# Kernel optimization log

Measured on AMD Instinct MI355X. Metric: run time of the kernel, lower is better.

Reference implementation:

```python
import jax, jax.numpy as jnp
import numpy as np

B, S, D, H = 2, 2048, 1024, 16
DK = D // H


def setup_inputs() -> dict:
    key = jax.random.key(0)
    ks = jax.random.split(key, 11)
    s = 1.0 / np.sqrt(D)
    inp = {
        "q": jax.random.normal(ks[0], (B, S, D), jnp.float32),
        "k": jax.random.normal(ks[1], (B, S, D), jnp.float32),
        "v": jax.random.normal(ks[2], (B, S, D), jnp.float32),
        "mask": jnp.tril(jnp.ones((S, S), jnp.int32))[None, None],  # causal [1,1,S,S]
        "w_q": jax.random.normal(ks[3], (D, D), jnp.float32) * s,
        "b_q": jax.random.normal(ks[4], (D,), jnp.float32) * 0.01,
        "w_k": jax.random.normal(ks[5], (D, D), jnp.float32) * s,
        "b_k": jax.random.normal(ks[6], (D,), jnp.float32) * 0.01,
        "w_v": jax.random.normal(ks[7], (D, D), jnp.float32) * s,
        "b_v": jax.random.normal(ks[8], (D,), jnp.float32) * 0.01,
        "w_o": jax.random.normal(ks[9], (D, D), jnp.float32) * s,
        "b_o": jax.random.normal(ks[10], (D,), jnp.float32) * 0.01,
    }
    return inp


def reference(q, k, v, mask, w_q, b_q, w_k, b_k, w_v, b_v, w_o, b_o):
    # Linear projections (torch Linear: x @ W.T + b)
    query = q @ w_q.T + b_q  # [B,S,D]
    key_ = k @ w_k.T + b_k
    value = v @ w_v.T + b_v
    # split heads -> [B,H,S,DK]
    def split(x):
        return x.reshape(B, S, H, DK).transpose(0, 2, 1, 3)
    qh, kh, vh = split(query), split(key_), split(value)
    scores = jnp.einsum("bhqd,bhkd->bhqk", qh, kh) / jnp.sqrt(jnp.float32(DK))
    scores = jnp.where(mask == 0, jnp.float32(-1e9), scores)
    attn = jax.nn.softmax(scores, axis=-1)
    out = jnp.einsum("bhqk,bhkd->bhqd", attn, vh)  # [B,H,S,DK]
    out = out.transpose(0, 2, 1, 3).reshape(B, S, D)
    return out @ w_o.T + b_o
```

## Files before the change

kernel.cpp:

```cpp
#include <hip/hip_runtime.h>


typedef __attribute__((ext_vector_type(8))) short bf16x8;
typedef __attribute__((ext_vector_type(4))) float floatx4;
typedef __attribute__((ext_vector_type(4))) unsigned short u16x4;

#define S_LEN 2048
#define D_MODEL 1024
#define N_HEADS 16
#define D_HEAD 64
#define M_ROWS 4096
#define QSCALE 0.18033688011112042f

__device__ __forceinline__ unsigned short f32_to_bf16(float f) {
  unsigned int u = __builtin_bit_cast(unsigned int, f);
  u += 0x7FFFu + ((u >> 16) & 1u);
  return (unsigned short)(u >> 16);
}

__global__ __launch_bounds__(256) void cvt_w(
    const float* __restrict__ w0, const float* __restrict__ w1,
    const float* __restrict__ w2, const float* __restrict__ w3,
    unsigned short* __restrict__ dst) {
  const int z = blockIdx.y;
  const float* src = (z == 0) ? w0 : (z == 1) ? w1 : (z == 2) ? w2 : w3;
  unsigned short* d = dst + ((long)z << 20);
  const int n4 = 1 << 18;
  for (int i = blockIdx.x * 256 + threadIdx.x; i < n4; i += gridDim.x * 256) {
    float4 f = ((const float4*)src)[i];
    u16x4 o;
    o[0] = f32_to_bf16(f.x); o[1] = f32_to_bf16(f.y);
    o[2] = f32_to_bf16(f.z); o[3] = f32_to_bf16(f.w);
    ((u16x4*)d)[i] = o;
  }
}

__global__ __launch_bounds__(256) void cvt_x(
    const float* __restrict__ x0, const float* __restrict__ x1,
    const float* __restrict__ x2, unsigned short* __restrict__ dst) {
  const int z = blockIdx.y;
  const float* src = (z == 0) ? x0 : (z == 1) ? x1 : x2;
  unsigned short* d = dst + (long)z * M_ROWS * D_MODEL;
  const int n4 = (M_ROWS * D_MODEL) / 4;
  for (int i = blockIdx.x * 256 + threadIdx.x; i < n4; i += gridDim.x * 256) {
    float4 f = ((const float4*)src)[i];
    u16x4 o;
    o[0] = f32_to_bf16(f.x); o[1] = f32_to_bf16(f.y);
    o[2] = f32_to_bf16(f.z); o[3] = f32_to_bf16(f.w);
    ((u16x4*)d)[i] = o;
  }
}

#define GK 1024
#define GN 1024
#define LDP 72

template <bool XPRE>
__global__ __launch_bounds__(256, 3) void qkv_gemm(
    const float* __restrict__ Xq, const float* __restrict__ Xk, const float* __restrict__ Xv,
    const unsigned short* __restrict__ Xb,
    const unsigned short* __restrict__ Wb,
    const float* __restrict__ bq, const float* __restrict__ bk, const float* __restrict__ bv,
    unsigned short* __restrict__ Yq, unsigned short* __restrict__ Yk,
    unsigned short* __restrict__ Yvt) {
  __shared__ __align__(16) unsigned short As[128 * LDP];
  __shared__ __align__(16) unsigned short Bs[128 * LDP];

  const int z = blockIdx.z;
  const unsigned short* W = Wb + ((long)z << 20);
  const float* bias = (z == 0) ? bq : ((z == 1) ? bk : bv);

  const int r0 = blockIdx.x * 128;
  const int n0 = blockIdx.y * 128;
  const int tid = threadIdx.x;
  const int lane = tid & 63;
  const int wave = tid >> 6;
  const int quad = lane >> 4;
  const int ln = lane & 15;
  const int wm = (wave >> 1) * 64;
  const int wn = (wave & 1) * 64;

  floatx4 acc[4][4];
#pragma unroll
  for (int i = 0; i < 4; i++)
#pragma unroll
    for (int j = 0; j < 4; j++) acc[i][j] = (floatx4){0.f, 0.f, 0.f, 0.f};

  const int srow = tid >> 1;
  const int scol = (tid & 1) * 32;
  unsigned short* Asw = As + srow * LDP + scol;
  unsigned short* Bsw = Bs + srow * LDP + scol;
  const unsigned short* Bp = W + (long)(n0 + srow) * GK + scol;
  const float* ApF = nullptr;
  const unsigned short* ApH = nullptr;
  if constexpr (XPRE) {
    ApH = Xb + (long)z * M_ROWS * D_MODEL + (long)(r0 + srow) * GK + scol;
  } else {
    const float* X = (z == 0) ? Xq : ((z == 1) ? Xk : Xv);
    ApF = X + (long)(r0 + srow) * GK + scol;
  }

  for (int k0 = 0; k0 < GK; k0 += 64) {
    float4 b0 = *(const float4*)(Bp + k0);
    float4 b1 = *(const float4*)(Bp + k0 + 8);
    float4 b2 = *(const float4*)(Bp + k0 + 16);
    float4 b3 = *(const float4*)(Bp + k0 + 24);
    float4 a0, a1, a2, a3;
    if constexpr (XPRE) {
      a0 = *(const float4*)(ApH + k0);
      a1 = *(const float4*)(ApH + k0 + 8);
      a2 = *(const float4*)(ApH + k0 + 16);
      a3 = *(const float4*)(ApH + k0 + 24);
    } else {
      unsigned short ua[32] __attribute__((aligned(16)));
      float fa[32] __attribute__((aligned(16)));
#pragma unroll
      for (int c = 0; c < 8; c++)
        *(float4*)(fa + c * 4) = *(const float4*)(ApF + k0 + c * 4);
#pragma unroll
      for (int j = 0; j < 32; j++) ua[j] = f32_to_bf16(fa[j]);
      a0 = *(float4*)(ua); a1 = *(float4*)(ua + 8);
      a2 = *(float4*)(ua + 16); a3 = *(float4*)(ua + 24);
    }
    __syncthreads();
    *(float4*)(Asw) = a0;      *(float4*)(Asw + 8) = a1;
    *(float4*)(Asw + 16) = a2; *(float4*)(Asw + 24) = a3;
    *(float4*)(Bsw) = b0;      *(float4*)(Bsw + 8) = b1;
    *(float4*)(Bsw + 16) = b2; *(float4*)(Bsw + 24) = b3;
    __syncthreads();

#pragma unroll
    for (int ks = 0; ks < 64; ks += 32) {
      bf16x8 af[4], bfr[4];
#pragma unroll
      for (int mt = 0; mt < 4; mt++)
        af[mt] = *(const bf16x8*)(As + (wm + mt * 16 + ln) * LDP + ks + quad * 8);
#pragma unroll
      for (int nt = 0; nt < 4; nt++)
        bfr[nt] = *(const bf16x8*)(Bs + (wn + nt * 16 + ln) * LDP + ks + quad * 8);
#pragma unroll
      for (int mt = 0; mt < 4; mt++)
#pragma unroll
        for (int nt = 0; nt < 4; nt++)
          acc[mt][nt] = __builtin_amdgcn_mfma_f32_16x16x32_bf16(af[mt], bfr[nt], acc[mt][nt], 0, 0, 0);
    }
  }

#pragma unroll
  for (int nt = 0; nt < 4; nt++) {
    const int n = n0 + wn + nt * 16 + ln;
    const float bv = bias[n];
#pragma unroll
    for (int mt = 0; mt < 4; mt++) {
      const int r = r0 + wm + mt * 16 + quad * 4;
      if (z == 2) {
        u16x4 pk;
#pragma unroll
        for (int reg = 0; reg < 4; reg++) pk[reg] = f32_to_bf16(acc[mt][nt][reg] + bv);
        *(u16x4*)(Yvt + (long)n * M_ROWS + r) = pk;
      } else if (z == 0) {
#pragma unroll
        for (int reg = 0; reg < 4; reg++)
          Yq[(long)(r + reg) * GN + n] = f32_to_bf16((acc[mt][nt][reg] + bv) * QSCALE);
      } else {
#pragma unroll
        for (int reg = 0; reg < 4; reg++)
          Yk[(long)(r + reg) * GN + n] = f32_to_bf16(acc[mt][nt][reg] + bv);
      }
    }
  }
}

__global__ __launch_bounds__(256, 3) void out_gemm(
    const unsigned short* __restrict__ X,
    const unsigned short* __restrict__ W,
    const float* __restrict__ bias,
    float* __restrict__ Y) {
  __shared__ __align__(16) unsigned short As[64 * LDP];
  __shared__ __align__(16) unsigned short Bs[128 * LDP];

  const int r0 = blockIdx.x * 64;
  const int n0 = blockIdx.y * 128;
  const int tid = threadIdx.x;
  const int lane = tid & 63;
  const int wave = tid >> 6;
  const int quad = lane >> 4;
  const int ln = lane & 15;
  const int wm = (wave >> 1) * 32;
  const int wn = (wave & 1) * 64;

  floatx4 acc[2][4];
#pragma unroll
  for (int i = 0; i < 2; i++)
#pragma unroll
    for (int j = 0; j < 4; j++) acc[i][j] = (floatx4){0.f, 0.f, 0.f, 0.f};

  const int arow = tid >> 2;
  const int acol = (tid & 3) * 16;
  const unsigned short* Ap = X + (long)(r0 + arow) * GK + acol;
  unsigned short* Asw = As + arow * LDP + acol;
  const int brow = tid >> 1;
  const int bcol = (tid & 1) * 32;
  const unsigned short* Bp = W + (long)(n0 + brow) * GK + bcol;
  unsigned short* Bsw = Bs + brow * LDP + bcol;

  for (int k0 = 0; k0 < GK; k0 += 64) {
    float4 a0 = *(const float4*)(Ap + k0);
    float4 a1 = *(const float4*)(Ap + k0 + 8);
    float4 b0 = *(const float4*)(Bp + k0);
    float4 b1 = *(const float4*)(Bp + k0 + 8);
    float4 b2 = *(const float4*)(Bp + k0 + 16);
    float4 b3 = *(const float4*)(Bp + k0 + 24);
    __syncthreads();
    *(float4*)(Asw) = a0;      *(float4*)(Asw + 8) = a1;
    *(float4*)(Bsw) = b0;      *(float4*)(Bsw + 8) = b1;
    *(float4*)(Bsw + 16) = b2; *(float4*)(Bsw + 24) = b3;
    __syncthreads();

#pragma unroll
    for (int ks = 0; ks < 64; ks += 32) {
      bf16x8 af[2], bfr[4];
#pragma unroll
      for (int mt = 0; mt < 2; mt++)
        af[mt] = *(const bf16x8*)(As + (wm + mt * 16 + ln) * LDP + ks + quad * 8);
#pragma unroll
      for (int nt = 0; nt < 4; nt++)
        bfr[nt] = *(const bf16x8*)(Bs + (wn + nt * 16 + ln) * LDP + ks + quad * 8);
#pragma unroll
      for (int mt = 0; mt < 2; mt++)
#pragma unroll
        for (int nt = 0; nt < 4; nt++)
          acc[mt][nt] = __builtin_amdgcn_mfma_f32_16x16x32_bf16(af[mt], bfr[nt], acc[mt][nt], 0, 0, 0);
    }
  }

#pragma unroll
  for (int nt = 0; nt < 4; nt++) {
    const int n = n0 + wn + nt * 16 + ln;
    const float bv = bias[n];
#pragma unroll
    for (int mt = 0; mt < 2; mt++) {
      const int r = r0 + wm + mt * 16 + quad * 4;
#pragma unroll
      for (int reg = 0; reg < 4; reg++)
        Y[(long)(r + reg) * GN + n] = acc[mt][nt][reg] + bv;
    }
  }
}

#define PSTR 72

__global__ __launch_bounds__(64, 2) void attn_causal(
    const unsigned short* __restrict__ Q,
    const unsigned short* __restrict__ K,
    const unsigned short* __restrict__ Vt,
    unsigned short* __restrict__ O) {
  __shared__ __align__(16) unsigned short PbA[16 * PSTR];
  __shared__ __align__(16) unsigned short PbB[16 * PSTR];

  const int bh = blockIdx.x;
  const int pr = blockIdx.y;
  const int b = bh >> 4;
  const int h = bh & 15;

  const int lane = threadIdx.x;
  const int quad = lane >> 4;
  const int ln = lane & 15;

  const int s1 = pr, s2 = 127 - pr;
  const int q0A = s1 * 16, q0B = s2 * 16;
  const int nkt1 = (s1 >> 2) + 1;
  const int nkt2 = (s2 >> 2) + 1;

  const unsigned short* Qb = Q + (long)b * S_LEN * D_MODEL + h * D_HEAD;
  const unsigned short* Kb = K + (long)b * S_LEN * D_MODEL + h * D_HEAD;
  const unsigned short* Vb = Vt + (long)h * D_HEAD * M_ROWS + b * S_LEN;

  bf16x8 qfA[2], qfB[2];
  qfA[0] = *(const bf16x8*)(Qb + (long)(q0A + ln) * D_MODEL + quad * 8);
  qfA[1] = *(const bf16x8*)(Qb + (long)(q0A + ln) * D_MODEL + 32 + quad * 8);
  qfB[0] = *(const bf16x8*)(Qb + (long)(q0B + ln) * D_MODEL + quad * 8);
  qfB[1] = *(const bf16x8*)(Qb + (long)(q0B + ln) * D_MODEL + 32 + quad * 8);

  float mA = -1e30f, lA = 0.f, mB = -1e30f, lB = 0.f;
  floatx4 oA[4], oB[4];
#pragma unroll
  for (int nt = 0; nt < 4; nt++) {
    oA[nt] = (floatx4){0.f, 0.f, 0.f, 0.f};
    oB[nt] = (floatx4){0.f, 0.f, 0.f, 0.f};
  }

  auto loadKV = [&](bf16x8 (&kf)[4][2], bf16x8 (&vf)[4][2], int kt) {
    const int kv0 = kt * 64;
#pragma unroll
    for (int ct = 0; ct < 4; ct++) {
      const unsigned short* kp = Kb + (long)(kv0 + ct * 16 + ln) * D_MODEL + quad * 8;
      kf[ct][0] = *(const bf16x8*)(kp);
      kf[ct][1] = *(const bf16x8*)(kp + 32);
      const unsigned short* vp = Vb + (long)(ct * 16 + ln) * M_ROWS + kv0 + quad * 8;
      vf[ct][0] = *(const bf16x8*)(vp);
      vf[ct][1] = *(const bf16x8*)(vp + 32);
    }
  };

  auto iter = [&](bf16x8 (&kf)[4][2], bf16x8 (&vf)[4][2], int kt) {
    const int kv0 = kt * 64;
    const bool aAct = (kt < nkt1);

    floatx4 sB[4], sA[4];
#pragma unroll
    for (int ct = 0; ct < 4; ct++) {
      sB[ct] = (floatx4){0.f, 0.f, 0.f, 0.f};
      sB[ct] = __builtin_amdgcn_mfma_f32_16x16x32_bf16(kf[ct][0], qfB[0], sB[ct], 0, 0, 0);
      sB[ct] = __builtin_amdgcn_mfma_f32_16x16x32_bf16(kf[ct][1], qfB[1], sB[ct], 0, 0, 0);
    }
    if (aAct) {
#pragma unroll
      for (int ct = 0; ct < 4; ct++) {
        sA[ct] = (floatx4){0.f, 0.f, 0.f, 0.f};
        sA[ct] = __builtin_amdgcn_mfma_f32_16x16x32_bf16(kf[ct][0], qfA[0], sA[ct], 0, 0, 0);
        sA[ct] = __builtin_amdgcn_mfma_f32_16x16x32_bf16(kf[ct][1], qfA[1], sA[ct], 0, 0, 0);
      }
    }

    {
      float tmax = -1e30f;
      if (kt == nkt2 - 1) {
        const int qg = q0B + ln;
#pragma unroll
        for (int ct = 0; ct < 4; ct++) {
          const int kvb = kv0 + ct * 16 + quad * 4;
#pragma unroll
          for (int reg = 0; reg < 4; reg++) {
            float sv = sB[ct][reg];
            if (kvb + reg > qg) sv = -1e30f;
            sB[ct][reg] = sv;
            tmax = fmaxf(tmax, sv);
          }
        }
      } else {
#pragma unroll
        for (int ct = 0; ct < 4; ct++)
#pragma unroll
          for (int reg = 0; reg < 4; reg++) tmax = fmaxf(tmax, sB[ct][reg]);
      }
      tmax = fmaxf(tmax, __shfl_xor(tmax, 16, 64));
      tmax = fmaxf(tmax, __shfl_xor(tmax, 32, 64));
      const float mnew = fmaxf(mB, tmax);
      const float alpha = exp2f(mB - mnew);
      mB = mnew;
      float rsum = 0.f;
#pragma unroll
      for (int ct = 0; ct < 4; ct++) {
        u16x4 pk;
#pragma unroll
        for (int reg = 0; reg < 4; reg++) {
          const float p = exp2f(sB[ct][reg] - mB);
          rsum += p;
          pk[reg] = f32_to_bf16(p);
        }
        *(u16x4*)(PbB + ln * PSTR + ct * 16 + quad * 4) = pk;
      }
      rsum += __shfl_xor(rsum, 16, 64);
      rsum += __shfl_xor(rsum, 32, 64);
      lB = lB * alpha + rsum;
#pragma unroll
      for (int nt = 0; nt < 4; nt++)
#pragma unroll
        for (int reg = 0; reg < 4; reg++) oB[nt][reg] *= alpha;
    }

    if (aAct) {
      float tmax = -1e30f;
      if (kt == nkt1 - 1) {
        const int qg = q0A + ln;
#pragma unroll
        for (int ct = 0; ct < 4; ct++) {
          const int kvb = kv0 + ct * 16 + quad * 4;
#pragma unroll
          for (int reg = 0; reg < 4; reg++) {
            float sv = sA[ct][reg];
            if (kvb + reg > qg) sv = -1e30f;
            sA[ct][reg] = sv;
            tmax = fmaxf(tmax, sv);
          }
        }
      } else {
#pragma unroll
        for (int ct = 0; ct < 4; ct++)
#pragma unroll
          for (int reg = 0; reg < 4; reg++) tmax = fmaxf(tmax, sA[ct][reg]);
      }
      tmax = fmaxf(tmax, __shfl_xor(tmax, 16, 64));
      tmax = fmaxf(tmax, __shfl_xor(tmax, 32, 64));
      const float mnew = fmaxf(mA, tmax);
      const float alpha = exp2f(mA - mnew);
      mA = mnew;
      float rsum = 0.f;
#pragma unroll
      for (int ct = 0; ct < 4; ct++) {
        u16x4 pk;
#pragma unroll
        for (int reg = 0; reg < 4; reg++) {
          const float p = exp2f(sA[ct][reg] - mA);
          rsum += p;
          pk[reg] = f32_to_bf16(p);
        }
        *(u16x4*)(PbA + ln * PSTR + ct * 16 + quad * 4) = pk;
      }
      rsum += __shfl_xor(rsum, 16, 64);
      rsum += __shfl_xor(rsum, 32, 64);
      lA = lA * alpha + rsum;
#pragma unroll
      for (int nt = 0; nt < 4; nt++)
#pragma unroll
        for (int reg = 0; reg < 4; reg++) oA[nt][reg] *= alpha;
    }

    __builtin_amdgcn_wave_barrier();

    {
      bf16x8 p0 = *(const bf16x8*)(PbB + ln * PSTR + quad * 8);
      bf16x8 p1 = *(const bf16x8*)(PbB + ln * PSTR + 32 + quad * 8);
#pragma unroll
      for (int nt = 0; nt < 4; nt++) {
        oB[nt] = __builtin_amdgcn_mfma_f32_16x16x32_bf16(vf[nt][0], p0, oB[nt], 0, 0, 0);
        oB[nt] = __builtin_amdgcn_mfma_f32_16x16x32_bf16(vf[nt][1], p1, oB[nt], 0, 0, 0);
      }
    }
    if (aAct) {
      bf16x8 p0 = *(const bf16x8*)(PbA + ln * PSTR + quad * 8);
      bf16x8 p1 = *(const bf16x8*)(PbA + ln * PSTR + 32 + quad * 8);
#pragma unroll
      for (int nt = 0; nt < 4; nt++) {
        oA[nt] = __builtin_amdgcn_mfma_f32_16x16x32_bf16(vf[nt][0], p0, oA[nt], 0, 0, 0);
        oA[nt] = __builtin_amdgcn_mfma_f32_16x16x32_bf16(vf[nt][1], p1, oA[nt], 0, 0, 0);
      }
    }
    __builtin_amdgcn_wave_barrier();
  };

  bf16x8 kf0[4][2], vf0[4][2], kf1[4][2], vf1[4][2];
  loadKV(kf0, vf0, 0);
#pragma unroll 1
  for (int kt = 0; kt < nkt2; kt += 2) {
    if (kt + 1 < nkt2) loadKV(kf1, vf1, kt + 1);
    iter(kf0, vf0, kt);
    if (kt + 1 >= nkt2) break;
    if (kt + 2 < nkt2) loadKV(kf0, vf0, kt + 2);
    iter(kf1, vf1, kt + 1);
  }

  {
    const float inv = 1.0f / lA;
    unsigned short* op = O + (long)b * S_LEN * D_MODEL + (long)(q0A + ln) * D_MODEL + h * D_HEAD;
#pragma unroll
    for (int nt = 0; nt < 4; nt++) {
      u16x4 pk;
#pragma unroll
      for (int reg = 0; reg < 4; reg++) pk[reg] = f32_to_bf16(oA[nt][reg] * inv);
      *(u16x4*)(op + nt * 16 + quad * 4) = pk;
    }
  }
  {
    const float inv = 1.0f / lB;
    unsigned short* op = O + (long)b * S_LEN * D_MODEL + (long)(q0B + ln) * D_MODEL + h * D_HEAD;
#pragma unroll
    for (int nt = 0; nt < 4; nt++) {
      u16x4 pk;
#pragma unroll
      for (int reg = 0; reg < 4; reg++) pk[reg] = f32_to_bf16(oB[nt][reg] * inv);
      *(u16x4*)(op + nt * 16 + quad * 4) = pk;
    }
  }
}

extern "C" void kernel_launch(void* const* d_in, const int* in_sizes, int n_in,
                              void* d_out, int out_size, void* d_ws, size_t ws_size,
                              hipStream_t stream) {
  const float* q = (const float*)d_in[0];
  const float* k = (const float*)d_in[1];
  const float* v = (const float*)d_in[2];
  const float* w_q = (const float*)d_in[4];
  const float* b_q = (const float*)d_in[5];
  const float* w_k = (const float*)d_in[6];
  const float* b_k = (const float*)d_in[7];
  const float* w_v = (const float*)d_in[8];
  const float* b_v = (const float*)d_in[9];
  const float* w_o = (const float*)d_in[10];
  const float* b_o = (const float*)d_in[11];
  float* out = (float*)d_out;

  unsigned short* ws = (unsigned short*)d_ws;
  const long NE = (long)M_ROWS * D_MODEL;
  const bool xpre = (ws_size >= (size_t)7 * NE * sizeof(unsigned short));

  unsigned short *Qp, *Kp, *Vpt, *AO, *Wb, *Xb;
  if (xpre) {
    Qp = ws;
    Kp = ws + NE;
    Vpt = ws + 2 * NE;
    Wb = ws + 3 * NE;
    Xb = ws + 4 * NE;
    AO = ws + 4 * NE;
  } else {
    Qp = ws;
    Kp = ws + NE;
    Vpt = ws + 2 * NE;
    AO = ws + 3 * NE;
    Wb = ws + 4 * NE;
    Xb = nullptr;
  }

  cvt_w<<<dim3(256, 4), 256, 0, stream>>>(w_q, w_k, w_v, w_o, Wb);
  if (xpre) {
    cvt_x<<<dim3(512, 3), 256, 0, stream>>>(q, k, v, Xb);
    qkv_gemm<true><<<dim3(M_ROWS / 128, GN / 128, 3), 256, 0, stream>>>(
        q, k, v, Xb, Wb, b_q, b_k, b_v, Qp, Kp, Vpt);
  } else {
    qkv_gemm<false><<<dim3(M_ROWS / 128, GN / 128, 3), 256, 0, stream>>>(
        q, k, v, nullptr, Wb, b_q, b_k, b_v, Qp, Kp, Vpt);
  }
  attn_causal<<<dim3(2 * N_HEADS, 64), 64, 0, stream>>>(Qp, Kp, Vpt, AO);
  out_gemm<<<dim3(M_ROWS / 64, GN / 128), 256, 0, stream>>>(AO, Wb + 3 * (1 << 20), b_o, out);
}
```

Measured before the change: 284.1 us.

## Split causal attention KV range across two waves with LDS softmax merge

Each attention block now runs two waves. Each wave processes half of the KV tiles for both query strips, and the partial outputs are combined through shared memory using a log-sum-exp merge. This doubles the number of waves working per query pair, which is meant to improve latency hiding and occupancy. The loop is also restructured to process each strip separately, prefetching K one tile ahead and loading V after the score MFMAs. The cost is extra LDS traffic, a block-wide barrier and merge arithmetic at the end.

Result: slower. 409.6 us (+44.2%).

```diff
diff --git a/kernel.cpp b/kernel.cpp
--- a/kernel.cpp
+++ b/kernel.cpp
@@ -249,21 +249,24 @@
 }
 
 #define PSTR 72
-
-__global__ __launch_bounds__(64, 2) void attn_causal(
+#define MSTR 20
+
+__global__ __launch_bounds__(128, 4) void attn_causal(
     const unsigned short* __restrict__ Q,
     const unsigned short* __restrict__ K,
     const unsigned short* __restrict__ Vt,
     unsigned short* __restrict__ O) {
-  __shared__ __align__(16) unsigned short PbA[16 * PSTR];
-  __shared__ __align__(16) unsigned short PbB[16 * PSTR];
+  __shared__ __align__(16) unsigned short Pb[2][16 * PSTR];
+  __shared__ __align__(16) float Mb[2][64 * MSTR];
 
   const int bh = blockIdx.x;
   const int pr = blockIdx.y;
   const int b = bh >> 4;
   const int h = bh & 15;
 
-  const int lane = threadIdx.x;
+  const int tid = threadIdx.x;
+  const int wave = tid >> 6;
+  const int lane = tid & 63;
   const int quad = lane >> 4;
   const int ln = lane & 15;
 
@@ -271,16 +274,14 @@
   const int q0A = s1 * 16, q0B = s2 * 16;
   const int nkt1 = (s1 >> 2) + 1;
   const int nkt2 = (s2 >> 2) + 1;
+  const int h1 = nkt1 >> 1;
+  const int h2 = nkt2 >> 1;
 
   const unsigned short* Qb = Q + (long)b * S_LEN * D_MODEL + h * D_HEAD;
   const unsigned short* Kb = K + (long)b * S_LEN * D_MODEL + h * D_HEAD;
   const unsigned short* Vb = Vt + (long)h * D_HEAD * M_ROWS + b * S_LEN;
 
-  bf16x8 qfA[2], qfB[2];
-  qfA[0] = *(const bf16x8*)(Qb + (long)(q0A + ln) * D_MODEL + quad * 8);
-  qfA[1] = *(const bf16x8*)(Qb + (long)(q0A + ln) * D_MODEL + 32 + quad * 8);
-  qfB[0] = *(const bf16x8*)(Qb + (long)(q0B + ln) * D_MODEL + quad * 8);
-  qfB[1] = *(const bf16x8*)(Qb + (long)(q0B + ln) * D_MODEL + 32 + quad * 8);
+  unsigned short* myP = Pb[wave];
 
   float mA = -1e30f, lA = 0.f, mB = -1e30f, lB = 0.f;
   floatx4 oA[4], oB[4];
@@ -290,51 +291,59 @@
     oB[nt] = (floatx4){0.f, 0.f, 0.f, 0.f};
   }
 
-  auto loadKV = [&](bf16x8 (&kf)[4][2], bf16x8 (&vf)[4][2], int kt) {
-    const int kv0 = kt * 64;
-#pragma unroll
-    for (int ct = 0; ct < 4; ct++) {
-      const unsigned short* kp = Kb + (long)(kv0 + ct * 16 + ln) * D_MODEL + quad * 8;
-      kf[ct][0] = *(const bf16x8*)(kp);
-      kf[ct][1] = *(const bf16x8*)(kp + 32);
-      const unsigned short* vp = Vb + (long)(ct * 16 + ln) * M_ROWS + kv0 + quad * 8;
-      vf[ct][0] = *(const bf16x8*)(vp);
-      vf[ct][1] = *(const bf16x8*)(vp + 32);
-    }
-  };
-
-  auto iter = [&](bf16x8 (&kf)[4][2], bf16x8 (&vf)[4][2], int kt) {
-    const int kv0 = kt * 64;
-    const bool aAct = (kt < nkt1);
-
-    floatx4 sB[4], sA[4];
-#pragma unroll
-    for (int ct = 0; ct < 4; ct++) {
-      sB[ct] = (floatx4){0.f, 0.f, 0.f, 0.f};
-      sB[ct] = __builtin_amdgcn_mfma_f32_16x16x32_bf16(kf[ct][0], qfB[0], sB[ct], 0, 0, 0);
-      sB[ct] = __builtin_amdgcn_mfma_f32_16x16x32_bf16(kf[ct][1], qfB[1], sB[ct], 0, 0, 0);
-    }
-    if (aAct) {
+  auto runStrip = [&](int q0, int lo, int hi, int nkt,
+                      floatx4 (&o)[4], float& m, float& l) {
+    if (lo >= hi) return;
+    bf16x8 qf[2];
+    qf[0] = *(const bf16x8*)(Qb + (long)(q0 + ln) * D_MODEL + quad * 8);
+    qf[1] = *(const bf16x8*)(Qb + (long)(q0 + ln) * D_MODEL + 32 + quad * 8);
+
+    bf16x8 kf0[4][2], kf1[4][2], vf[4][2];
+
+    auto loadK = [&](bf16x8 (&kf)[4][2], int kt) {
+      const int kv0 = kt * 64;
 #pragma unroll
       for (int ct = 0; ct < 4; ct++) {
-        sA[ct] = (floatx4){0.f, 0.f, 0.f, 0.f};
-        sA[ct] = __builtin_amdgcn_mfma_f32_16x16x32_bf16(kf[ct][0], qfA[0], sA[ct], 0, 0, 0);
-        sA[ct] = __builtin_amdgcn_mfma_f32_16x16x32_bf16(kf[ct][1], qfA[1], sA[ct], 0, 0, 0);
-      }
-    }
-
-    {
+        const unsigned short* kp = Kb + (long)(kv0 + ct * 16 + ln) * D_MODEL + quad * 8;
+        kf[ct][0] = *(const bf16x8*)(kp);
+        kf[ct][1] = *(const bf16x8*)(kp + 32);
+      }
+    };
+    auto loadV = [&](int kt) {
+      const int kv0 = kt * 64;
+#pragma unroll
+      for (int ct = 0; ct < 4; ct++) {
+        const unsigned short* vp = Vb + (long)(ct * 16 + ln) * M_ROWS + kv0 + quad * 8;
+        vf[ct][0] = *(const bf16x8*)(vp);
+        vf[ct][1] = *(const bf16x8*)(vp + 32);
+      }
+    };
+
+    auto iter = [&](bf16x8 (&kf)[4][2], int kt, bool pre, bf16x8 (&kfn)[4][2]) {
+      const int kv0 = kt * 64;
+
+      floatx4 s[4];
+#pragma unroll
+      for (int ct = 0; ct < 4; ct++) {
+        s[ct] = (floatx4){0.f, 0.f, 0.f, 0.f};
+        s[ct] = __builtin_amdgcn_mfma_f32_16x16x32_bf16(kf[ct][0], qf[0], s[ct], 0, 0, 0);
+        s[ct] = __builtin_amdgcn_mfma_f32_16x16x32_bf16(kf[ct][1], qf[1], s[ct], 0, 0, 0);
+      }
+
+      loadV(kt);
+      if (pre) loadK(kfn, kt + 1);
+
       float tmax = -1e30f;
-      if (kt == nkt2 - 1) {
-        const int qg = q0B + ln;
+      if (kt == nkt - 1) {
+        const int qg = q0 + ln;
 #pragma unroll
         for (int ct = 0; ct < 4; ct++) {
           const int kvb = kv0 + ct * 16 + quad * 4;
 #pragma unroll
           for (int reg = 0; reg < 4; reg++) {
-            float sv = sB[ct][reg];
+            float sv = s[ct][reg];
             if (kvb + reg > qg) sv = -1e30f;
-            sB[ct][reg] = sv;
+            s[ct][reg] = sv;
             tmax = fmaxf(tmax, sv);
           }
         }
@@ -342,137 +351,92 @@
 #pragma unroll
         for (int ct = 0; ct < 4; ct++)
 #pragma unroll
-          for (int reg = 0; reg < 4; reg++) tmax = fmaxf(tmax, sB[ct][reg]);
+          for (int reg = 0; reg < 4; reg++) tmax = fmaxf(tmax, s[ct][reg]);
       }
       tmax = fmaxf(tmax, __shfl_xor(tmax, 16, 64));
       tmax = fmaxf(tmax, __shfl_xor(tmax, 32, 64));
-      const float mnew = fmaxf(mB, tmax);
-      const float alpha = exp2f(mB - mnew);
-      mB = mnew;
+      const float mnew = fmaxf(m, tmax);
+      const float alpha = exp2f(m - mnew);
+      m = mnew;
       float rsum = 0.f;
 #pragma unroll
       for (int ct = 0; ct < 4; ct++) {
         u16x4 pk;
 #pragma unroll
         for (int reg = 0; reg < 4; reg++) {
-          const float p = exp2f(sB[ct][reg] - mB);
+          const float p = exp2f(s[ct][reg] - m);
           rsum += p;
           pk[reg] = f32_to_bf16(p);
         }
-        *(u16x4*)(PbB + ln * PSTR + ct * 16 + quad * 4) = pk;
+        *(u16x4*)(myP + ln * PSTR + ct * 16 + quad * 4) = pk;
       }
       rsum += __shfl_xor(rsum, 16, 64);
       rsum += __shfl_xor(rsum, 32, 64);
-      lB = lB * alpha + rsum;
+      l = l * alpha + rsum;
 #pragma unroll
       for (int nt = 0; nt < 4; nt++)
 #pragma unroll
-        for (int reg = 0; reg < 4; reg++) oB[nt][reg] *= alpha;
-    }
-
-    if (aAct) {
-      float tmax = -1e30f;
-      if (kt == nkt1 - 1) {
-        const int qg = q0A + ln;
-#pragma unroll
-        for (int ct = 0; ct < 4; ct++) {
-          const int kvb = kv0 + ct * 16 + quad * 4;
-#pragma unroll
-          for (int reg = 0; reg < 4; reg++) {
-            float sv = sA[ct][reg];
-            if (kvb + reg > qg) sv = -1e30f;
-            sA[ct][reg] = sv;
-            tmax = fmaxf(tmax, sv);
-          }
-        }
-      } else {
-#pragma unroll
-        for (int ct = 0; ct < 4; ct++)
-#pragma unroll
-          for (int reg = 0; reg < 4; reg++) tmax = fmaxf(tmax, sA[ct][reg]);
-      }
-      tmax = fmaxf(tmax, __shfl_xor(tmax, 16, 64));
-      tmax = fmaxf(tmax, __shfl_xor(tmax, 32, 64));
-      const float mnew = fmaxf(mA, tmax);
-      const float alpha = exp2f(mA - mnew);
-      mA = mnew;
-      float rsum = 0.f;
-#pragma unroll
-      for (int ct = 0; ct < 4; ct++) {
-        u16x4 pk;
-#pragma unroll
-        for (int reg = 0; reg < 4; reg++) {
-          const float p = exp2f(sA[ct][reg] - mA);
-          rsum += p;
-          pk[reg] = f32_to_bf16(p);
-        }
-        *(u16x4*)(PbA + ln * PSTR + ct * 16 + quad * 4) = pk;
-      }
-      rsum += __shfl_xor(rsum, 16, 64);
-      rsum += __shfl_xor(rsum, 32, 64);
-      lA = lA * alpha + rsum;
-#pragma unroll
-      for (int nt = 0; nt < 4; nt++)
-#pragma unroll
-        for (int reg = 0; reg < 4; reg++) oA[nt][reg] *= alpha;
-    }
-
-    __builtin_amdgcn_wave_barrier();
-
-    {
-      bf16x8 p0 = *(const bf16x8*)(PbB + ln * PSTR + quad * 8);
-      bf16x8 p1 = *(const bf16x8*)(PbB + ln * PSTR + 32 + quad * 8);
+        for (int reg = 0; reg < 4; reg++) o[nt][reg] *= alpha;
+
+      __builtin_amdgcn_wave_barrier();
+
+      bf16x8 p0 = *(const bf16x8*)(myP + ln * PSTR + quad * 8);
+      bf16x8 p1 = *(const bf16x8*)(myP + ln * PSTR + 32 + quad * 8);
 #pragma unroll
       for (int nt = 0; nt < 4; nt++) {
-        oB[nt] = __builtin_amdgcn_mfma_f32_16x16x32_bf16(vf[nt][0], p0, oB[nt], 0, 0, 0);
-        oB[nt] = __builtin_amdgcn_mfma_f32_16x16x32_bf16(vf[nt][1], p1, oB[nt], 0, 0, 0);
-      }
-    }
-    if (aAct) {
-      bf16x8 p0 = *(const bf16x8*)(PbA + ln * PSTR + quad * 8);
-      bf16x8 p1 = *(const bf16x8*)(PbA + ln * PSTR + 32 + quad * 8);
-#pragma unroll
-      for (int nt = 0; nt < 4; nt++) {
-        oA[nt] = __builtin_amdgcn_mfma_f32_16x16x32_bf16(vf[nt][0], p0, oA[nt], 0, 0, 0);
-        oA[nt] = __builtin_amdgcn_mfma_f32_16x16x32_bf16(vf[nt][1], p1, oA[nt], 0, 0, 0);
-      }
-    }
-    __builtin_amdgcn_wave_barrier();
+        o[nt] = __builtin_amdgcn_mfma_f32_16x16x32_bf16(vf[nt][0], p0, o[nt], 0, 0, 0);
+        o[nt] = __builtin_amdgcn_mfma_f32_16x16x32_bf16(vf[nt][1], p1, o[nt], 0, 0, 0);
+      }
+      __builtin_amdgcn_wave_barrier();
+    };
+
+    loadK(kf0, lo);
+#pragma unroll 1
+    for (int kt = lo; kt < hi; kt += 2) {
+      iter(kf0, kt, kt + 1 < hi, kf1);
+      if (kt + 1 >= hi) break;
+      iter(kf1, kt + 1, kt + 2 < hi, kf0);
+    }
   };
 
-  bf16x8 kf0[4][2], vf0[4][2], kf1[4][2], vf1[4][2];
-  loadKV(kf0, vf0, 0);
-#pragma unroll 1
-  for (int kt = 0; kt < nkt2; kt += 2) {
-    if (kt + 1 < nkt2) loadKV(kf1, vf1, kt + 1);
-    iter(kf0, vf0, kt);
-    if (kt + 1 >= nkt2) break;
-    if (kt + 2 < nkt2) loadKV(kf0, vf0, kt + 2);
-    iter(kf1, vf1, kt + 1);
-  }
-
-  {
-    const float inv = 1.0f / lA;
-    unsigned short* op = O + (long)b * S_LEN * D_MODEL + (long)(q0A + ln) * D_MODEL + h * D_HEAD;
+  const int loA = wave ? h1 : 0, hiA = wave ? nkt1 : h1;
+  const int loB = wave ? h2 : 0, hiB = wave ? nkt2 : h2;
+  runStrip(q0A, loA, hiA, nkt1, oA, mA, lA);
+  runStrip(q0B, loB, hiB, nkt2, oB, mB, lB);
+
+  auto storePartial = [&](floatx4 (&o)[4], float m, float l) {
+    float* mb = &Mb[wave][lane * MSTR];
+    *(floatx4*)(mb + 0) = o[0];
+    *(floatx4*)(mb + 4) = o[1];
+    *(floatx4*)(mb + 8) = o[2];
+    *(floatx4*)(mb + 12) = o[3];
+    mb[16] = m;
+    mb[17] = l;
+  };
+  auto mergeOut = [&](floatx4 (&o)[4], float m, float l, int q0) {
+    const float* ob = &Mb[1 - wave][lane * MSTR];
+    const float m1 = ob[16], l1 = ob[17];
+    const float M = fmaxf(m, m1);
+    const float w0 = exp2f(m - M);
+    const float w1 = exp2f(m1 - M);
+    const float inv = 1.0f / (l * w0 + l1 * w1);
+    unsigned short* op = O + (long)b * S_LEN * D_MODEL + (long)(q0 + ln) * D_MODEL + h * D_HEAD;
 #pragma unroll
     for (int nt = 0; nt < 4; nt++) {
+      const floatx4 o1 = *(const floatx4*)(ob + nt * 4);
       u16x4 pk;
 #pragma unroll
-      for (int reg = 0; reg < 4; reg++) pk[reg] = f32_to_bf16(oA[nt][reg] * inv);
+      for (int reg = 0; reg < 4; reg++)
+        pk[reg] = f32_to_bf16((o[nt][reg] * w0 + o1[reg] * w1) * inv);
       *(u16x4*)(op + nt * 16 + quad * 4) = pk;
     }
-  }
-  {
-    const float inv = 1.0f / lB;
-    unsigned short* op = O + (long)b * S_LEN * D_MODEL + (long)(q0B + ln) * D_MODEL + h * D_HEAD;
-#pragma unroll
-    for (int nt = 0; nt < 4; nt++) {
-      u16x4 pk;
-#pragma unroll
-      for (int reg = 0; reg < 4; reg++) pk[reg] = f32_to_bf16(oB[nt][reg] * inv);
-      *(u16x4*)(op + nt * 16 + quad * 4) = pk;
-    }
-  }
+  };
+
+  if (wave == 0) storePartial(oB, mB, lB);
+  else           storePartial(oA, mA, lA);
+  __syncthreads();
+  if (wave == 0) mergeOut(oA, mA, lA, q0A);
+  else           mergeOut(oB, mB, lB, q0B);
 }
 
 extern "C" void kernel_launch(void* const* d_in, const int* in_sizes, int n_in,
@@ -521,6 +485,6 @@
     qkv_gemm<false><<<dim3(M_ROWS / 128, GN / 128, 3), 256, 0, stream>>>(
         q, k, v, nullptr, Wb, b_q, b_k, b_v, Qp, Kp, Vpt);
   }
-  attn_causal<<<dim3(2 * N_HEADS, 64), 64, 0, stream>>>(Qp, Kp, Vpt, AO);
+  attn_causal<<<dim3(2 * N_HEADS, 64), 128, 0, stream>>>(Qp, Kp, Vpt, AO);
   out_gemm<<<dim3(M_ROWS / 64, GN / 128), 256, 0, stream>>>(AO, Wb + 3 * (1 << 20), b_o, out);
 }
```

## Split attention KV loop across two waves with LDS softmax merge

Applied to the files above, without the earlier changes.

The causal attention block grows from one wave to two. Each wave handles alternating KV tiles (interleaved stride), and both partial online-softmax states are merged through shared memory at the end, with each wave writing one of the two query tiles. The aim is more parallelism per query pair and shorter serial KV loops, to hide latency. The cost is extra LDS for per-wave P buffers and the merge buffer, a block barrier, and more combine work.

Measured after the change: 287.7 us. About the same (+1.3%).

```diff
diff --git a/kernel.cpp b/kernel.cpp
--- a/kernel.cpp
+++ b/kernel.cpp
@@ -249,21 +249,25 @@
 }
 
 #define PSTR 72
-
-__global__ __launch_bounds__(64, 2) void attn_causal(
+#define MSTR 20
+
+__global__ __launch_bounds__(128, 2) void attn_causal(
     const unsigned short* __restrict__ Q,
     const unsigned short* __restrict__ K,
     const unsigned short* __restrict__ Vt,
     unsigned short* __restrict__ O) {
-  __shared__ __align__(16) unsigned short PbA[16 * PSTR];
-  __shared__ __align__(16) unsigned short PbB[16 * PSTR];
+  __shared__ __align__(16) unsigned short PbA[2][16 * PSTR];
+  __shared__ __align__(16) unsigned short PbB[2][16 * PSTR];
+  __shared__ __align__(16) float Mb[2][64 * MSTR];
 
   const int bh = blockIdx.x;
   const int pr = blockIdx.y;
   const int b = bh >> 4;
   const int h = bh & 15;
 
-  const int lane = threadIdx.x;
+  const int tid = threadIdx.x;
+  const int wave = tid >> 6;
+  const int lane = tid & 63;
   const int quad = lane >> 4;
   const int ln = lane & 15;
 
@@ -275,6 +279,9 @@
   const unsigned short* Qb = Q + (long)b * S_LEN * D_MODEL + h * D_HEAD;
   const unsigned short* Kb = K + (long)b * S_LEN * D_MODEL + h * D_HEAD;
   const unsigned short* Vb = Vt + (long)h * D_HEAD * M_ROWS + b * S_LEN;
+
+  unsigned short* myPA = PbA[wave];
+  unsigned short* myPB = PbB[wave];
 
   bf16x8 qfA[2], qfB[2];
   qfA[0] = *(const bf16x8*)(Qb + (long)(q0A + ln) * D_MODEL + quad * 8);
@@ -359,7 +366,7 @@
           rsum += p;
           pk[reg] = f32_to_bf16(p);
         }
-        *(u16x4*)(PbB + ln * PSTR + ct * 16 + quad * 4) = pk;
+        *(u16x4*)(myPB + ln * PSTR + ct * 16 + quad * 4) = pk;
       }
       rsum += __shfl_xor(rsum, 16, 64);
       rsum += __shfl_xor(rsum, 32, 64);
@@ -406,7 +413,7 @@
           rsum += p;
           pk[reg] = f32_to_bf16(p);
         }
-        *(u16x4*)(PbA + ln * PSTR + ct * 16 + quad * 4) = pk;
+        *(u16x4*)(myPA + ln * PSTR + ct * 16 + quad * 4) = pk;
       }
       rsum += __shfl_xor(rsum, 16, 64);
       rsum += __shfl_xor(rsum, 32, 64);
@@ -420,8 +427,8 @@
     __builtin_amdgcn_wave_barrier();
 
     {
-      bf16x8 p0 = *(const bf16x8*)(PbB + ln * PSTR + quad * 8);
-      bf16x8 p1 = *(const bf16x8*)(PbB + ln * PSTR + 32 + quad * 8);
+      bf16x8 p0 = *(const bf16x8*)(myPB + ln * PSTR + quad * 8);
+      bf16x8 p1 = *(const bf16x8*)(myPB + ln * PSTR + 32 + quad * 8);
 #pragma unroll
       for (int nt = 0; nt < 4; nt++) {
         oB[nt] = __builtin_amdgcn_mfma_f32_16x16x32_bf16(vf[nt][0], p0, oB[nt], 0, 0, 0);
@@ -429,8 +436,8 @@
       }
     }
     if (aAct) {
-      bf16x8 p0 = *(const bf16x8*)(PbA + ln * PSTR + quad * 8);
-      bf16x8 p1 = *(const bf16x8*)(PbA + ln * PSTR + 32 + quad * 8);
+      bf16x8 p0 = *(const bf16x8*)(myPA + ln * PSTR + quad * 8);
+      bf16x8 p1 = *(const bf16x8*)(myPA + ln * PSTR + 32 + quad * 8);
 #pragma unroll
       for (int nt = 0; nt < 4; nt++) {
         oA[nt] = __builtin_amdgcn_mfma_f32_16x16x32_bf16(vf[nt][0], p0, oA[nt], 0, 0, 0);
@@ -441,35 +448,66 @@
   };
 
   bf16x8 kf0[4][2], vf0[4][2], kf1[4][2], vf1[4][2];
-  loadKV(kf0, vf0, 0);
+  loadKV(kf0, vf0, wave);
 #pragma unroll 1
-  for (int kt = 0; kt < nkt2; kt += 2) {
-    if (kt + 1 < nkt2) loadKV(kf1, vf1, kt + 1);
+  for (int kt = wave; kt < nkt2; kt += 4) {
+    if (kt + 2 < nkt2) loadKV(kf1, vf1, kt + 2);
     iter(kf0, vf0, kt);
-    if (kt + 1 >= nkt2) break;
-    if (kt + 2 < nkt2) loadKV(kf0, vf0, kt + 2);
-    iter(kf1, vf1, kt + 1);
-  }
-
-  {
-    const float inv = 1.0f / lA;
+    if (kt + 2 >= nkt2) break;
+    if (kt + 4 < nkt2) loadKV(kf0, vf0, kt + 4);
+    iter(kf1, vf1, kt + 2);
+  }
+
+  if (wave == 0) {
+    float* mb = &Mb[0][lane * MSTR];
+    *(floatx4*)(mb + 0) = oB[0];
+    *(floatx4*)(mb + 4) = oB[1];
+    *(floatx4*)(mb + 8) = oB[2];
+    *(floatx4*)(mb + 12) = oB[3];
+    mb[16] = mB;
+    mb[17] = lB;
+  } else {
+    float* mb = &Mb[1][lane * MSTR];
+    *(floatx4*)(mb + 0) = oA[0];
+    *(floatx4*)(mb + 4) = oA[1];
+    *(floatx4*)(mb + 8) = oA[2];
+    *(floatx4*)(mb + 12) = oA[3];
+    mb[16] = mA;
+    mb[17] = lA;
+  }
+  __syncthreads();
+  if (wave == 0) {
+    const float* ob = &Mb[1][lane * MSTR];
+    const float m1 = ob[16], l1 = ob[17];
+    const float M = fmaxf(mA, m1);
+    const float w0 = exp2f(mA - M);
+    const float w1 = exp2f(m1 - M);
+    const float inv = 1.0f / (lA * w0 + l1 * w1);
     unsigned short* op = O + (long)b * S_LEN * D_MODEL + (long)(q0A + ln) * D_MODEL + h * D_HEAD;
 #pragma unroll
     for (int nt = 0; nt < 4; nt++) {
+      const floatx4 o1 = *(const floatx4*)(ob + nt * 4);
       u16x4 pk;
 #pragma unroll
-      for (int reg = 0; reg < 4; reg++) pk[reg] = f32_to_bf16(oA[nt][reg] * inv);
+      for (int reg = 0; reg < 4; reg++)
+        pk[reg] = f32_to_bf16((oA[nt][reg] * w0 + o1[reg] * w1) * inv);
       *(u16x4*)(op + nt * 16 + quad * 4) = pk;
     }
-  }
-  {
-    const float inv = 1.0f / lB;
+  } else {
+    const float* ob = &Mb[0][lane * MSTR];
+    const float m1 = ob[16], l1 = ob[17];
+    const float M = fmaxf(mB, m1);
+    const float w0 = exp2f(mB - M);
+    const float w1 = exp2f(m1 - M);
+    const float inv = 1.0f / (lB * w0 + l1 * w1);
     unsigned short* op = O + (long)b * S_LEN * D_MODEL + (long)(q0B + ln) * D_MODEL + h * D_HEAD;
 #pragma unroll
     for (int nt = 0; nt < 4; nt++) {
+      const floatx4 o1 = *(const floatx4*)(ob + nt * 4);
       u16x4 pk;
 #pragma unroll
-      for (int reg = 0; reg < 4; reg++) pk[reg] = f32_to_bf16(oB[nt][reg] * inv);
+      for (int reg = 0; reg < 4; reg++)
+        pk[reg] = f32_to_bf16((oB[nt][reg] * w0 + o1[reg] * w1) * inv);
       *(u16x4*)(op + nt * 16 + quad * 4) = pk;
     }
   }
@@ -521,6 +559,6 @@
     qkv_gemm<false><<<dim3(M_ROWS / 128, GN / 128, 3), 256, 0, stream>>>(
         q, k, v, nullptr, Wb, b_q, b_k, b_v, Qp, Kp, Vpt);
   }
-  attn_causal<<<dim3(2 * N_HEADS, 64), 64, 0, stream>>>(Qp, Kp, Vpt, AO);
+  attn_causal<<<dim3(2 * N_HEADS, 64), 128, 0, stream>>>(Qp, Kp, Vpt, AO);
   out_gemm<<<dim3(M_ROWS / 64, GN / 128), 256, 0, stream>>>(AO, Wb + 3 * (1 << 20), b_o, out);
 }
```
